# Kernel optimization log

Measured on AMD Instinct MI355X. Metric: run time of the kernel, lower is better.

The kernel has to match this reference:

```python
import jax, jax.numpy as jnp
import numpy as np

B, H, W, C, F = 32, 32, 32, 256, 64
K_NEIGH = 32  # L1 pixel-distance cutoff used for the static mask


def _distance_mask(h, w, k):
    # coords: [hw, 2] of (y, x); L1 pixel distances, normalized by max(h, w)
    ys, xs = jnp.meshgrid(jnp.arange(h), jnp.arange(w), indexing='ij')
    coords = jnp.stack([ys, xs], axis=-1).reshape(-1, 2).astype(jnp.float32)
    diff = jnp.abs(coords[:, None, :] - coords[None, :, :]).sum(-1)  # [hw, hw], == cdist p=1
    dist = diff / float(max(h, w))
    return jnp.where(diff <= k, dist, 0.0)


def setup_inputs() -> dict:
    key = jax.random.key(0)
    ks = jax.random.split(key, 7)
    return {
        'feature_map': jax.random.normal(ks[0], (B, H, W, C), dtype=jnp.float32),
        'emb_W': jax.random.normal(ks[1], (F, C), dtype=jnp.float32) * (1.0 / np.sqrt(C)),
        'emb_b': jax.random.normal(ks[2], (F,), dtype=jnp.float32) * 0.01,
        'attn_W': jax.random.normal(ks[3], (C, C), dtype=jnp.float32) * (1.0 / np.sqrt(C)),
        'attn_b': jax.random.normal(ks[4], (C,), dtype=jnp.float32) * 0.01,
        'thr_W': jax.random.normal(ks[5], (1, C), dtype=jnp.float32) * (1.0 / np.sqrt(C)),
        'thr_b': jax.random.normal(ks[6], (1,), dtype=jnp.float32) * 0.01,
        'layer': 0,
    }


def reference(feature_map, emb_W, emb_b, attn_W, attn_b, thr_W, thr_b, layer):
    b, h, w, c = feature_map.shape
    hw = h * w
    x = feature_map.reshape(b, hw, c)  # row-major (y, x) flatten, matches torch view

    # 1x1 conv -> per-pixel linear: instance embeddings [b, hw, F]
    emb = jnp.einsum('bnc,fc->bnf', x, emb_W) + emb_b

    # squared Euclidean pairwise distances (cdist p=2, then squared)
    sq = jnp.sum(emb * emb, axis=-1)  # [b, hw]
    d2 = jnp.maximum(sq[:, :, None] + sq[:, None, :]
                     - 2.0 * jnp.einsum('bnf,bmf->bnm', emb, emb), 0.0)

    mask = _distance_mask(h, w, K_NEIGH)  # [hw, hw] static buffer
    sim = jax.nn.softmax(jnp.exp(-d2) - (1.0 - mask), axis=-1)  # [b, hw, hw]

    # shortcut = attention_conv(feature_map): [b, hw, c]
    shortcut = jnp.einsum('bnc,dc->bnd', x, attn_W) + attn_b

    # per-pixel learned threshold: [b, hw]
    Tinst = (jnp.einsum('bnc,oc->bno', shortcut, thr_W) + thr_b)[..., 0]

    A = jax.nn.softmax(jnp.maximum(sim - Tinst[:, None, :], 0.0), axis=-1)

    # bmm: out[b, i, c] = sum_j shortcut[b, j, c] * A[b, i, j]
    attn_out = jnp.einsum('bjc,bij->bic', shortcut, A)

    res = (x + attn_out).reshape(b, h, w, c)
    return res
```

## Files before the change

### kernel.cpp

```cpp
#include <hip/hip_runtime.h>
#include <hip/hip_bf16.h>


typedef short bf16x8 __attribute__((ext_vector_type(8)));
typedef float f32x4 __attribute__((ext_vector_type(4)));

__device__ __forceinline__ unsigned short f2bf(float f) {
  unsigned u = __float_as_uint(f);
  u += 0x7fffu + ((u >> 16) & 1u);
  return (unsigned short)(u >> 16);
}
__device__ __forceinline__ float bf2f(unsigned short h) {
  return __uint_as_float(((unsigned)h) << 16);
}
__device__ __forceinline__ f32x4 mfma16(bf16x8 a, bf16x8 b, f32x4 c) {
  return __builtin_amdgcn_mfma_f32_16x16x32_bf16(a, b, c, 0, 0, 0);
}
__device__ __forceinline__ int iabs(int v) { return v < 0 ? -v : v; }
__device__ __forceinline__ void load_lds16(const void* g, void* l) {
  __builtin_amdgcn_global_load_lds(
      (const __attribute__((address_space(1))) unsigned int*)g,
      (__attribute__((address_space(3))) unsigned int*)l, 16, 0, 0);
}

__global__ __launch_bounds__(256) void k_prep(const float* __restrict__ x,
                                              const float* __restrict__ embW,
                                              const float* __restrict__ attnW,
                                              unsigned short* __restrict__ xb,
                                              unsigned short* __restrict__ Wb) {
  const int tid = blockIdx.x * 256 + threadIdx.x;
  {
    float4 v = *(const float4*)(x + (size_t)tid * 4);
    ushort4 p; p.x = f2bf(v.x); p.y = f2bf(v.y); p.z = f2bf(v.z); p.w = f2bf(v.w);
    *(ushort4*)(xb + (size_t)tid * 4) = p;
  }
  if (tid < 81920) {
    float v = (tid < 16384) ? embW[tid] : attnW[tid - 16384];
    Wb[tid] = f2bf(v);
  }
}

__global__ __launch_bounds__(256) void k_lin(const unsigned short* __restrict__ xb,
                                             const unsigned short* __restrict__ Wb,
                                             const float* __restrict__ embB,
                                             const float* __restrict__ attnB,
                                             const float* __restrict__ thrW,
                                             const float* __restrict__ thrB,
                                             unsigned short* __restrict__ embb,
                                             float* __restrict__ sq,
                                             unsigned short* __restrict__ scT,
                                             float* __restrict__ Tout) {
  __shared__ union {
    struct { unsigned short xs[64][40]; unsigned short ws[320][40]; } a;
    unsigned short St[256][72];
  } sm;
  const int t = threadIdx.x;
  const int Mbase = blockIdx.x * 64;
  const int lane = t & 63, wave = t >> 6;
  const int wm = wave >> 1, wn = wave & 1;
  const int l15 = lane & 15, quad = lane >> 4;

  f32x4 acc[2][10] = {};
  for (int k0 = 0; k0 < 256; k0 += 32) {
    {
      int row = t >> 2, c0 = (t & 3) * 8;
      *(uint4*)&sm.a.xs[row][c0] =
          *(const uint4*)(xb + (size_t)(Mbase + row) * 256 + k0 + c0);
    }
    {
      const unsigned short* wsrc = Wb + (size_t)t * 256 + k0;
      for (int s = 0; s < 4; s++)
        *(uint4*)&sm.a.ws[t][s * 8] = *(const uint4*)(wsrc + s * 8);
      if (t < 64) {
        const unsigned short* wsrc2 = Wb + (size_t)(256 + t) * 256 + k0;
        for (int s = 0; s < 4; s++)
          *(uint4*)&sm.a.ws[256 + t][s * 8] = *(const uint4*)(wsrc2 + s * 8);
      }
    }
    __syncthreads();
    bf16x8 af[2];
    af[0] = *(const bf16x8*)&sm.a.xs[wm * 32 + l15][quad * 8];
    af[1] = *(const bf16x8*)&sm.a.xs[wm * 32 + 16 + l15][quad * 8];
    for (int nt = 0; nt < 10; nt++) {
      bf16x8 bfr = *(const bf16x8*)&sm.a.ws[wn * 160 + nt * 16 + l15][quad * 8];
      acc[0][nt] = mfma16(af[0], bfr, acc[0][nt]);
      acc[1][nt] = mfma16(af[1], bfr, acc[1][nt]);
    }
    __syncthreads();
  }

  if (wn == 0) {
    float sp[2][4] = {{0.f,0.f,0.f,0.f},{0.f,0.f,0.f,0.f}};
    for (int rt = 0; rt < 2; rt++)
      for (int nt = 0; nt < 4; nt++) {
        int n = nt * 16 + l15;
        float bias = embB[n];
        for (int r = 0; r < 4; r++) {
          float v = acc[rt][nt][r] + bias;
          unsigned short hb = f2bf(v);
          int row = wm * 32 + rt * 16 + quad * 4 + r;
          embb[(size_t)(Mbase + row) * 64 + n] = hb;
          float vf = bf2f(hb);
          sp[rt][r] += vf * vf;
        }
      }
    for (int m = 8; m >= 1; m >>= 1)
      for (int rt = 0; rt < 2; rt++)
        for (int r = 0; r < 4; r++)
          sp[rt][r] += __shfl_xor(sp[rt][r], m);
    if (l15 == 0)
      for (int rt = 0; rt < 2; rt++)
        for (int r = 0; r < 4; r++)
          sq[Mbase + wm * 32 + rt * 16 + quad * 4 + r] = sp[rt][r];
  }

  for (int rt = 0; rt < 2; rt++)
    for (int nt = 0; nt < 10; nt++) {
      int n = wn * 160 + nt * 16 + l15;
      if (n < 64) continue;
      int c = n - 64;
      float bias = attnB[c];
      for (int r = 0; r < 4; r++) {
        float v = acc[rt][nt][r] + bias;
        sm.St[c][wm * 32 + rt * 16 + quad * 4 + r] = f2bf(v);
      }
    }
  __syncthreads();

  const int b = Mbase >> 10, jbase = Mbase & 1023;
  {
    unsigned short* dst = scT + ((size_t)b * 256 + t) * 1024 + jbase;
    for (int s = 0; s < 8; s++)
      *(uint4*)(dst + s * 8) = *(const uint4*)&sm.St[t][s * 8];
  }
  {
    float tp = 0.f;
    int j = t >> 2, cs = (t & 3) * 64;
    for (int c = 0; c < 64; c++)
      tp += bf2f(sm.St[cs + c][j]) * thrW[cs + c];
    tp += __shfl_xor(tp, 1);
    tp += __shfl_xor(tp, 2);
    if ((t & 3) == 0) Tout[Mbase + j] = tp + thrB[0];
  }
}

__global__ __launch_bounds__(256) void k_scores(const unsigned short* __restrict__ embb,
                                                const float* __restrict__ sq,
                                                const float* __restrict__ T,
                                                unsigned short* __restrict__ U,
                                                float* __restrict__ Z) {
  __shared__ unsigned short E_lds[16 * 1040];
  __shared__ float rbuf[16];
  __shared__ float mtab[64];
  const int t = threadIdx.x, lane = t & 63, wave = t >> 6;
  const int b = blockIdx.x >> 6, rb = (blockIdx.x & 63) * 16;
  const int l15 = lane & 15, quad = lane >> 4;
  const unsigned short* eb = embb + (size_t)b * 1024 * 64;

  if (t < 16) rbuf[t] = 0.f;
  if (t < 64) {
    float m = (t <= 32) ? (float)t * (1.f / 32.f) : 0.f;
    mtab[t] = __expf(m - 1.f);
  }
  __syncthreads();

  const int rowA = rb + l15;
  bf16x8 a0 = *(const bf16x8*)(eb + (size_t)rowA * 64 + quad * 8);
  bf16x8 a1 = *(const bf16x8*)(eb + (size_t)rowA * 64 + 32 + quad * 8);
  const int rloc = quad * 4;
  float nsqi[4]; int yi[4], xi[4];
  for (int r = 0; r < 4; r++) {
    int rowg = rb + rloc + r;
    nsqi[r] = -sq[b * 1024 + rowg];
    yi[r] = rowg >> 5; xi[r] = rowg & 31;
  }
  const int jq = wave * 256;
  float rp[4] = {0.f, 0.f, 0.f, 0.f};
  for (int j0 = jq; j0 < jq + 256; j0 += 16) {
    const int jr = j0 + l15;
    bf16x8 b0 = *(const bf16x8*)(eb + (size_t)jr * 64 + quad * 8);
    bf16x8 b1 = *(const bf16x8*)(eb + (size_t)jr * 64 + 32 + quad * 8);
    f32x4 g = {0.f, 0.f, 0.f, 0.f};
    g = mfma16(a0, b0, g);
    g = mfma16(a1, b1, g);
    float sqj = sq[b * 1024 + jr];
    int yj = jr >> 5, xj = jr & 31;
    for (int r = 0; r < 4; r++) {
      float w = fminf(fmaf(2.f, g[r], nsqi[r] - sqj), 0.f);
      float v = __expf(w);
      int diff = iabs(yi[r] - yj) + iabs(xi[r] - xj);
      float e = __expf(v) * mtab[diff];
      E_lds[(rloc + r) * 1040 + jr] = f2bf(e);
      rp[r] += e;
    }
  }
  for (int m = 8; m >= 1; m >>= 1)
    for (int r = 0; r < 4; r++)
      rp[r] += __shfl_xor(rp[r], m);
  __syncthreads();
  if (l15 == 0)
    for (int r = 0; r < 4; r++)
      atomicAdd(&rbuf[rloc + r], rp[r]);
  __syncthreads();

  const int prow = t >> 4, seg = t & 15;
  const float invR = 1.f / rbuf[prow];
  const float* Tb = T + b * 1024;
  unsigned short* ur = U + ((size_t)(b * 1024 + rb + prow)) * 1024;
  float z = 0.f;
  for (int c = 0; c < 8; c++) {
    int j = c * 128 + seg * 8;
    union { bf16x8 v; unsigned short s[8]; } ev;
    ev.v = *(const bf16x8*)&E_lds[prow * 1040 + j];
    float4 t0 = *(const float4*)(Tb + j);
    float4 t1 = *(const float4*)(Tb + j + 4);
    float tf[8] = {t0.x, t0.y, t0.z, t0.w, t1.x, t1.y, t1.z, t1.w};
    union { uint4 v; unsigned short s[8]; } uo;
    for (int k = 0; k < 8; k++) {
      float u = __expf(fmaxf(fmaf(bf2f(ev.s[k]), invR, -tf[k]), 0.f));
      unsigned short h = f2bf(u);
      uo.s[k] = h;
      z += bf2f(h);
    }
    *(uint4*)(ur + j) = uo.v;
  }
  z += __shfl_xor(z, 1);
  z += __shfl_xor(z, 2);
  z += __shfl_xor(z, 4);
  z += __shfl_xor(z, 8);
  if (seg == 0) Z[b * 1024 + rb + prow] = z;
}

__global__ __launch_bounds__(256) void k_out(const unsigned short* __restrict__ U,
                                             const float* __restrict__ Z,
                                             const unsigned short* __restrict__ scT,
                                             const float* __restrict__ x,
                                             float* __restrict__ out) {
  __shared__ unsigned short Ab[128 * 32];
  __shared__ unsigned short Bb[128 * 32];
  const int t = threadIdx.x, lane = t & 63, wave = t >> 6;
  const int wm = wave >> 1, wn = wave & 1;
  const int l15 = lane & 15, quad = lane >> 4;
  const int x8 = blockIdx.x & 7, s = blockIdx.x >> 3;
  const int b = x8 * 4 + (s >> 4), tile = s & 15;
  const int rb = (tile >> 1) * 128, cb = (tile & 1) * 128;

  const unsigned short* Ubase = U + (size_t)b * 1024 * 1024 + (size_t)rb * 1024;
  const unsigned short* Sbase = scT + (size_t)b * 256 * 1024 + (size_t)cb * 1024;

  int c0 = wave * 64 + lane;
  int c1 = c0 + 256;
  const int r0 = c0 >> 2, o0 = (c0 & 3) * 8;
  const int r1 = c1 >> 2, o1 = (c1 & 3) * 8;

  f32x4 acc[4][4] = {};
  for (int j0 = 0; j0 < 1024; j0 += 32) {
    load_lds16(Ubase + (size_t)r0 * 1024 + j0 + o0, Ab + c0 * 8);
    load_lds16(Ubase + (size_t)r1 * 1024 + j0 + o1, Ab + c1 * 8);
    load_lds16(Sbase + (size_t)r0 * 1024 + j0 + o0, Bb + c0 * 8);
    load_lds16(Sbase + (size_t)r1 * 1024 + j0 + o1, Bb + c1 * 8);
    __syncthreads();
    bf16x8 af[4], bf[4];
    for (int i = 0; i < 4; i++)
      af[i] = *(const bf16x8*)&Ab[(wm * 64 + i * 16 + l15) * 32 + quad * 8];
    for (int i = 0; i < 4; i++)
      bf[i] = *(const bf16x8*)&Bb[(wn * 64 + i * 16 + l15) * 32 + quad * 8];
    for (int i = 0; i < 4; i++)
      for (int j = 0; j < 4; j++)
        acc[i][j] = mfma16(af[i], bf[j], acc[i][j]);
    __syncthreads();
  }

  const int colb = cb + wn * 64;
  for (int i = 0; i < 4; i++) {
    int rowb = rb + wm * 64 + i * 16 + quad * 4;
    float iz[4];
    for (int r = 0; r < 4; r++) iz[r] = 1.f / Z[b * 1024 + rowb + r];
    for (int j = 0; j < 4; j++) {
      int c = colb + j * 16 + l15;
      for (int r = 0; r < 4; r++) {
        size_t idx = ((size_t)(b * 1024 + rowb + r)) * 256 + c;
        out[idx] = x[idx] + acc[i][j][r] * iz[r];
      }
    }
  }
}

extern "C" void kernel_launch(void* const* d_in, const int* in_sizes, int n_in,
                              void* d_out, int out_size, void* d_ws, size_t ws_size,
                              hipStream_t stream) {
  const float* x     = (const float*)d_in[0];
  const float* embW  = (const float*)d_in[1];
  const float* embB  = (const float*)d_in[2];
  const float* attnW = (const float*)d_in[3];
  const float* attnB = (const float*)d_in[4];
  const float* thrW  = (const float*)d_in[5];
  const float* thrB  = (const float*)d_in[6];
  float* out = (float*)d_out;

  char* ws = (char*)d_ws;
  unsigned short* embb = (unsigned short*)(ws);
  unsigned short* scT  = (unsigned short*)(ws + (4ull << 20));
  unsigned short* U    = (unsigned short*)(ws + (20ull << 20));
  unsigned short* xb   = (unsigned short*)(ws + (20ull << 20));
  unsigned short* Wb   = (unsigned short*)(ws + (36ull << 20));
  float* sq = (float*)(ws + (84ull << 20));
  float* T  = (float*)(ws + (84ull << 20) + (128ull << 10));
  float* Z  = (float*)(ws + (84ull << 20) + (256ull << 10));

  k_prep<<<8192, 256, 0, stream>>>(x, embW, attnW, xb, Wb);
  k_lin<<<512, 256, 0, stream>>>(xb, Wb, embB, attnB, thrW, thrB, embb, sq, scT, T);
  k_scores<<<2048, 256, 0, stream>>>(embb, sq, T, U, Z);
  k_out<<<512, 256, 0, stream>>>(U, Z, scT, x, out);
}
```

Measured before the change: 198.8 us.

## Fuse input bf16 conversion into k_lin and widen k_scores to 512 threads

The prep kernel no longer converts the whole feature map to bf16; k_lin now reads fp32 input directly and packs it to bf16 while staging into LDS, removing a full write+read round trip of the activation tensor and shrinking the prep launch to weights only. k_scores now uses 8 waves per block, each covering 128 columns, and the epilogue uses 32 lanes per row, raising parallelism per 16-row tile. The mask index math is also simplified using the fact that the four rows share a y coordinate. k_lin loads twice as many bytes from global per tile, and the larger k_scores block may lower occupancy.

```diff
diff --git a/kernel.cpp b/kernel.cpp
--- a/kernel.cpp
+++ b/kernel.cpp
@@ -12,6 +12,9 @@
 }
 __device__ __forceinline__ float bf2f(unsigned short h) {
   return __uint_as_float(((unsigned)h) << 16);
+}
+__device__ __forceinline__ unsigned pack2(float a, float b) {
+  return (unsigned)f2bf(a) | ((unsigned)f2bf(b) << 16);
 }
 __device__ __forceinline__ f32x4 mfma16(bf16x8 a, bf16x8 b, f32x4 c) {
   return __builtin_amdgcn_mfma_f32_16x16x32_bf16(a, b, c, 0, 0, 0);
@@ -23,24 +26,17 @@
       (__attribute__((address_space(3))) unsigned int*)l, 16, 0, 0);
 }
 
-__global__ __launch_bounds__(256) void k_prep(const float* __restrict__ x,
-                                              const float* __restrict__ embW,
+__global__ __launch_bounds__(256) void k_prep(const float* __restrict__ embW,
                                               const float* __restrict__ attnW,
-                                              unsigned short* __restrict__ xb,
                                               unsigned short* __restrict__ Wb) {
-  const int tid = blockIdx.x * 256 + threadIdx.x;
-  {
-    float4 v = *(const float4*)(x + (size_t)tid * 4);
-    ushort4 p; p.x = f2bf(v.x); p.y = f2bf(v.y); p.z = f2bf(v.z); p.w = f2bf(v.w);
-    *(ushort4*)(xb + (size_t)tid * 4) = p;
-  }
-  if (tid < 81920) {
-    float v = (tid < 16384) ? embW[tid] : attnW[tid - 16384];
-    Wb[tid] = f2bf(v);
-  }
-}
-
-__global__ __launch_bounds__(256) void k_lin(const unsigned short* __restrict__ xb,
+  const int i = (blockIdx.x * 256 + threadIdx.x) * 4;
+  float4 v = (i < 16384) ? *(const float4*)(embW + i)
+                         : *(const float4*)(attnW + (i - 16384));
+  ushort4 p; p.x = f2bf(v.x); p.y = f2bf(v.y); p.z = f2bf(v.z); p.w = f2bf(v.w);
+  *(ushort4*)(Wb + i) = p;
+}
+
+__global__ __launch_bounds__(256) void k_lin(const float* __restrict__ x,
                                              const unsigned short* __restrict__ Wb,
                                              const float* __restrict__ embB,
                                              const float* __restrict__ attnB,
@@ -64,8 +60,12 @@
   for (int k0 = 0; k0 < 256; k0 += 32) {
     {
       int row = t >> 2, c0 = (t & 3) * 8;
-      *(uint4*)&sm.a.xs[row][c0] =
-          *(const uint4*)(xb + (size_t)(Mbase + row) * 256 + k0 + c0);
+      const float* src = x + (size_t)(Mbase + row) * 256 + k0 + c0;
+      float4 a = *(const float4*)src;
+      float4 b = *(const float4*)(src + 4);
+      uint4 p; p.x = pack2(a.x, a.y); p.y = pack2(a.z, a.w);
+      p.z = pack2(b.x, b.y); p.w = pack2(b.z, b.w);
+      *(uint4*)&sm.a.xs[row][c0] = p;
     }
     {
       const unsigned short* wsrc = Wb + (size_t)t * 256 + k0;
@@ -144,7 +144,7 @@
   }
 }
 
-__global__ __launch_bounds__(256) void k_scores(const unsigned short* __restrict__ embb,
+__global__ __launch_bounds__(512) void k_scores(const unsigned short* __restrict__ embb,
                                                 const float* __restrict__ sq,
                                                 const float* __restrict__ T,
                                                 unsigned short* __restrict__ U,
@@ -168,15 +168,12 @@
   bf16x8 a0 = *(const bf16x8*)(eb + (size_t)rowA * 64 + quad * 8);
   bf16x8 a1 = *(const bf16x8*)(eb + (size_t)rowA * 64 + 32 + quad * 8);
   const int rloc = quad * 4;
-  float nsqi[4]; int yi[4], xi[4];
-  for (int r = 0; r < 4; r++) {
-    int rowg = rb + rloc + r;
-    nsqi[r] = -sq[b * 1024 + rowg];
-    yi[r] = rowg >> 5; xi[r] = rowg & 31;
-  }
-  const int jq = wave * 256;
+  const int yi0 = (rb + rloc) >> 5, xi0 = (rb + rloc) & 31;
+  float nsqi[4];
+  for (int r = 0; r < 4; r++) nsqi[r] = -sq[b * 1024 + rb + rloc + r];
+  const int jq = wave * 128;
   float rp[4] = {0.f, 0.f, 0.f, 0.f};
-  for (int j0 = jq; j0 < jq + 256; j0 += 16) {
+  for (int j0 = jq; j0 < jq + 128; j0 += 16) {
     const int jr = j0 + l15;
     bf16x8 b0 = *(const bf16x8*)(eb + (size_t)jr * 64 + quad * 8);
     bf16x8 b1 = *(const bf16x8*)(eb + (size_t)jr * 64 + 32 + quad * 8);
@@ -184,11 +181,12 @@
     g = mfma16(a0, b0, g);
     g = mfma16(a1, b1, g);
     float sqj = sq[b * 1024 + jr];
-    int yj = jr >> 5, xj = jr & 31;
+    int dy = iabs(yi0 - (jr >> 5));
+    int dxa = xi0 - (jr & 31);
     for (int r = 0; r < 4; r++) {
       float w = fminf(fmaf(2.f, g[r], nsqi[r] - sqj), 0.f);
       float v = __expf(w);
-      int diff = iabs(yi[r] - yj) + iabs(xi[r] - xj);
+      int diff = dy + iabs(dxa + r);
       float e = __expf(v) * mtab[diff];
       E_lds[(rloc + r) * 1040 + jr] = f2bf(e);
       rp[r] += e;
@@ -203,13 +201,13 @@
       atomicAdd(&rbuf[rloc + r], rp[r]);
   __syncthreads();
 
-  const int prow = t >> 4, seg = t & 15;
+  const int prow = t >> 5, seg = t & 31;
   const float invR = 1.f / rbuf[prow];
   const float* Tb = T + b * 1024;
   unsigned short* ur = U + ((size_t)(b * 1024 + rb + prow)) * 1024;
   float z = 0.f;
-  for (int c = 0; c < 8; c++) {
-    int j = c * 128 + seg * 8;
+  for (int c = 0; c < 4; c++) {
+    int j = c * 256 + seg * 8;
     union { bf16x8 v; unsigned short s[8]; } ev;
     ev.v = *(const bf16x8*)&E_lds[prow * 1040 + j];
     float4 t0 = *(const float4*)(Tb + j);
@@ -228,6 +226,7 @@
   z += __shfl_xor(z, 2);
   z += __shfl_xor(z, 4);
   z += __shfl_xor(z, 8);
+  z += __shfl_xor(z, 16);
   if (seg == 0) Z[b * 1024 + rb + prow] = z;
 }
 
@@ -302,14 +301,13 @@
   unsigned short* embb = (unsigned short*)(ws);
   unsigned short* scT  = (unsigned short*)(ws + (4ull << 20));
   unsigned short* U    = (unsigned short*)(ws + (20ull << 20));
-  unsigned short* xb   = (unsigned short*)(ws + (20ull << 20));
   unsigned short* Wb   = (unsigned short*)(ws + (36ull << 20));
   float* sq = (float*)(ws + (84ull << 20));
   float* T  = (float*)(ws + (84ull << 20) + (128ull << 10));
   float* Z  = (float*)(ws + (84ull << 20) + (256ull << 10));
 
-  k_prep<<<8192, 256, 0, stream>>>(x, embW, attnW, xb, Wb);
-  k_lin<<<512, 256, 0, stream>>>(xb, Wb, embB, attnB, thrW, thrB, embb, sq, scT, T);
-  k_scores<<<2048, 256, 0, stream>>>(embb, sq, T, U, Z);
+  k_prep<<<80, 256, 0, stream>>>(embW, attnW, Wb);
+  k_lin<<<512, 256, 0, stream>>>(x, Wb, embB, attnB, thrW, thrB, embb, sq, scT, T);
+  k_scores<<<2048, 512, 0, stream>>>(embb, sq, T, U, Z);
   k_out<<<512, 256, 0, stream>>>(U, Z, scT, x, out);
 }
```

New measurement: 195.4 us. About the same (-1.7%).
